# Kernel tuning notes

Measured on AMD Instinct MI355X. Metric: run time of the kernel, lower is better.

Reference implementation:

```python
import jax, jax.numpy as jnp
import numpy as np
import math

H, W = 512, 1024
PS = 2
H_p, W_p = H // PS, W // PS
N = 9
C_IN, C_OUT = 128, 64
GROUPS = 32
B = 2
EPS_GN = 1e-5


def _make_grid():
    # Replicates LatDeform2xDown buffers: centers + sec(lat)-scaled 3x3 offsets.
    pr = np.arange(H_p, dtype=np.float32) * PS + (PS - 1) / 2
    pc = np.arange(W_p, dtype=np.float32) * PS + (PS - 1) / 2
    cy = pr / (H - 1) * 2 - 1
    cx = pc / (W - 1) * 2 - 1
    centers = np.stack([np.broadcast_to(cx[None, :], (H_p, W_p)),
                        np.broadcast_to(cy[:, None], (H_p, W_p))], axis=-1)  # (H_p,W_p,2)
    delta = math.pi / (H - 1)  # drop_south_pole = False
    lat = math.pi / 2 - pr * delta
    sec_max = W / 4.0
    sec = np.clip(1.0 / np.cos(lat), -sec_max, sec_max).astype(np.float32)
    ky, kx = np.meshgrid(np.array([-1.0, 0.0, 1.0], np.float32),
                         np.array([-1.0, 0.0, 1.0], np.float32), indexing='ij')
    kxf, kyf = kx.flatten(), ky.flatten()
    dx = (kxf[None, :] * sec[:, None]) / (W - 1) * 2          # (H_p, 9)
    dy = np.broadcast_to(kyf[None, :], (H_p, N)) / (H - 1) * 2  # (H_p, 9)
    offsets = np.stack([dx, dy], axis=-1)                      # (H_p, 9, 2)
    locs = centers[:, :, None, :] + offsets[:, None, :, :]     # (H_p, W_p, 9, 2)
    return jnp.asarray(locs.reshape(-1, 2).astype(np.float32))


def group_norm(x, gamma, beta, groups, eps=EPS_GN):
    b, c, h, w = x.shape
    xg = x.reshape(b, groups, c // groups, h, w)
    mu = xg.mean(axis=(2, 3, 4), keepdims=True)
    var = ((xg - mu) ** 2).mean(axis=(2, 3, 4), keepdims=True)
    xn = ((xg - mu) * jax.lax.rsqrt(var + eps)).reshape(b, c, h, w)
    return xn * gamma[None, :, None, None] + beta[None, :, None, None]


def setup_inputs() -> dict:
    key = jax.random.key(0)
    ks = jax.random.split(key, 3)
    x = jax.random.normal(ks[0], (B, C_IN, H_p, W_p), dtype=jnp.float32)
    w_conv = jax.random.normal(ks[1], (N * C_OUT, C_IN), dtype=jnp.float32) * 0.02
    w_post = jax.random.normal(ks[2], (C_OUT, C_OUT), dtype=jnp.float32) * 0.05
    return {
        'x': x,
        'grid': _make_grid(),
        'gamma1': jnp.ones((C_IN,), jnp.float32),
        'beta1': jnp.zeros((C_IN,), jnp.float32),
        'w_conv': w_conv,
        'splat_bias': jnp.zeros((C_OUT,), jnp.float32),
        'w_post': w_post,
        'b_post': jnp.zeros((C_OUT,), jnp.float32),
        'gamma2': jnp.ones((C_OUT,), jnp.float32),
        'beta2': jnp.zeros((C_OUT,), jnp.float32),
    }


def reference(x, grid, gamma1, beta1, w_conv, splat_bias, w_post, b_post, gamma2, beta2):
    b = x.shape[0]
    # norm + 1x1 conv (no bias): Wx part of the Wx+b split
    h = group_norm(x, gamma1, beta1, GROUPS)
    vals = jnp.einsum('oc,bchw->bohw', w_conv, h)                 # (B, 9*C, H_p, W_p)
    vals = vals.reshape(b, C_OUT, N, H_p, W_p).transpose(0, 1, 3, 4, 2)
    vals = vals.reshape(b, C_OUT, H_p * W_p * N)                  # (B, C, M)

    # bilinear splat coordinates
    px = (grid[:, 0] + 1.0) * 0.5 * (W - 1)                       # (M,)
    py = (grid[:, 1] + 1.0) * 0.5 * (H - 1)
    x0 = jnp.floor(px).astype(jnp.int32)
    y0 = jnp.floor(py).astype(jnp.int32)
    x1, y1 = x0 + 1, y0 + 1
    fx = px - x0.astype(px.dtype)
    fy = py - y0.astype(py.dtype)
    w00 = (1 - fx) * (1 - fy)
    w01 = (1 - fx) * fy
    w10 = fx * (1 - fy)
    w11 = fx * fy
    x0w = x0 % W
    x1w = x1 % W
    half_W = W // 2

    def polar_wrap(yi, xi):
        past_n = yi < 0
        past_s = yi >= H
        yi = jnp.where(past_n, -yi, yi)
        yi = jnp.where(past_s, 2 * H - yi, yi)
        xi = jnp.where(past_n | past_s, (xi + half_W) % W, xi)
        return jnp.clip(yi, 0, H - 1), xi

    num = jnp.zeros((b, C_OUT, H * W), x.dtype)
    den = jnp.zeros((H * W,), x.dtype)  # identical across batch in the original
    for wt, yi, xi in ((w00, y0, x0w), (w01, y1, x0w), (w10, y0, x1w), (w11, y1, x1w)):
        yi, xi = polar_wrap(yi, xi)
        idx = yi * W + xi                                          # (M,)
        num = num.at[:, :, idx].add(vals * wt[None, None, :])
        den = den.at[idx].add(wt)

    out = num / jnp.clip(den, 1e-8)[None, None, :]
    out = out.reshape(b, C_OUT, H, W) + splat_bias[None, :, None, None]
    # post: 1x1 conv + GroupNorm + exact GELU
    out = jnp.einsum('oc,bchw->bohw', w_post, out) + b_post[None, :, None, None]
    out = group_norm(out, gamma2, beta2, GROUPS)
    return jax.nn.gelu(out, approximate=False)
```

## Files before the change

kernel.cpp:

```cpp
#include <hip/hip_runtime.h>
#include <cstdint>
#include <cstddef>

#define H_   512
#define W_   1024
#define HP_  256
#define WP_  512
#define NTAP 9
#define CIN  128
#define COUT 64
#define HWP  (HP_*WP_)
#define MIDX (HWP*NTAP)
#define HW_  (H_*W_)

typedef __attribute__((ext_vector_type(8))) short bhalf8_t;
typedef __attribute__((ext_vector_type(4))) float floatx4_t;

__device__ __forceinline__ unsigned short f2bf(float f) {
    unsigned u = __float_as_uint(f);
    u += 0x7fffu + ((u >> 16) & 1u);
    return (unsigned short)(u >> 16);
}
__device__ __forceinline__ float bf2f(unsigned short s) {
    return __uint_as_float(((unsigned)s) << 16);
}

__global__ __launch_bounds__(256) void k0_prep(
    const float* __restrict__ w_conv, const float* __restrict__ w_post,
    const float* __restrict__ sbias,  const float* __restrict__ b_post,
    unsigned short* __restrict__ w2, float* __restrict__ sb2,
    float* __restrict__ gnzero ) {
    int idx = blockIdx.x * 256 + threadIdx.x;
    if (idx < 73728) {
        int r = idx >> 7, ci = idx & 127;
        int n = r >> 6, o = r & 63;
        float acc = 0.f;
        #pragma unroll 8
        for (int op = 0; op < 64; ++op)
            acc = fmaf(w_post[o*64 + op], w_conv[(op*9 + n)*128 + ci], acc);
        w2[idx] = f2bf(acc);
    } else if (idx < 73728 + 64) {
        int o = idx - 73728;
        float acc = b_post[o];
        for (int op = 0; op < 64; ++op)
            acc = fmaf(w_post[o*64 + op], sbias[op], acc);
        sb2[o] = acc;
    } else if (idx < 73728 + 64 + 256) {
        gnzero[idx - (73728 + 64)] = 0.f;
    }
}

__global__ __launch_bounds__(256) void k1_stats(const float* __restrict__ x,
                                                float* __restrict__ gnsum1) {
    __shared__ float red[512];
    int bid = blockIdx.x;
    int b = bid >> 8, rem = bid & 255;
    int g = rem >> 3, slice = rem & 7;
    const float4* xp = (const float4*)x + (size_t)(b*CIN + g*4) * (HWP/4) + (size_t)slice*16384;
    float s = 0.f, s2 = 0.f;
    for (int i = threadIdx.x; i < 16384; i += 256) {
        float4 v = xp[i];
        s  += v.x + v.y + v.z + v.w;
        s2 += v.x*v.x + v.y*v.y + v.z*v.z + v.w*v.w;
    }
    red[threadIdx.x] = s; red[256 + threadIdx.x] = s2;
    __syncthreads();
    for (int off = 128; off > 0; off >>= 1) {
        if (threadIdx.x < off) {
            red[threadIdx.x] += red[threadIdx.x + off];
            red[256 + threadIdx.x] += red[256 + threadIdx.x + off];
        }
        __syncthreads();
    }
    if (threadIdx.x == 0) {
        atomicAdd(&gnsum1[(b*32 + g)*2],     red[0]);
        atomicAdd(&gnsum1[(b*32 + g)*2 + 1], red[256]);
    }
}

__global__ void k1b_coef(const float* __restrict__ gnsum1,
                         const float* __restrict__ gamma1, const float* __restrict__ beta1,
                         float* __restrict__ acoef, float* __restrict__ bcoef) {
    int t = threadIdx.x;
    int b = t >> 7, c = t & 127, g = c >> 2;
    float s1 = gnsum1[(b*32+g)*2], s2 = gnsum1[(b*32+g)*2+1];
    const float inv = 1.f / 524288.f;
    float mean = s1 * inv;
    float var  = s2 * inv - mean*mean;
    float rstd = rsqrtf(var + 1e-5f);
    float a = gamma1[c] * rstd;
    acoef[t] = a;
    bcoef[t] = beta1[c] - mean * a;
}

__global__ __launch_bounds__(256) void k2_conv(
    const float* __restrict__ x, const unsigned short* __restrict__ w2,
    const float* __restrict__ acoef, const float* __restrict__ bcoef,
    unsigned short* __restrict__ vals) {
    __shared__ unsigned short As[64*136];
    __shared__ unsigned short Bs[128*136];
    __shared__ unsigned short Cs[128*72];
    int b   = blockIdx.y;
    int tile = blockIdx.x;
    int pr  = tile >> 2, pcb = (tile & 3) << 7;
    int tid = threadIdx.x;

    for (int task = tid; task < 2048; task += 256) {
        int p = task & 127, c0 = (task >> 7) << 3;
        bhalf8_t t8;
        #pragma unroll
        for (int j = 0; j < 8; ++j) {
            int c = c0 + j;
            float xv = x[(size_t)(b*CIN + c)*HWP + (size_t)pr*WP_ + pcb + p];
            float v = fmaf(xv, acoef[b*CIN + c], bcoef[b*CIN + c]);
            t8[j] = (short)f2bf(v);
        }
        *(bhalf8_t*)&Bs[p*136 + c0] = t8;
    }
    __syncthreads();

    int wave = tid >> 6, lane = tid & 63;
    int l15 = lane & 15, lq = lane >> 4;

    bhalf8_t bfr[2][4];
    #pragma unroll
    for (int ptl = 0; ptl < 2; ++ptl) {
        int p = (wave*2 + ptl)*16 + l15;
        #pragma unroll
        for (int ks = 0; ks < 4; ++ks)
            bfr[ptl][ks] = *(const bhalf8_t*)&Bs[p*136 + ks*32 + lq*8];
    }

    for (int n = 0; n < 9; ++n) {
        __syncthreads();
        for (int i = tid; i < 4096; i += 256) {
            int r = i >> 6, cp = i & 63;
            ((unsigned*)As)[r*68 + cp] = ((const unsigned*)w2)[(n*64 + r)*64 + cp];
        }
        __syncthreads();
        floatx4_t acc[2][4] = {};
        #pragma unroll
        for (int ks = 0; ks < 4; ++ks) {
            bhalf8_t af[4];
            #pragma unroll
            for (int rt = 0; rt < 4; ++rt)
                af[rt] = *(const bhalf8_t*)&As[(rt*16 + l15)*136 + ks*32 + lq*8];
            #pragma unroll
            for (int ptl = 0; ptl < 2; ++ptl)
                #pragma unroll
                for (int rt = 0; rt < 4; ++rt)
                    acc[ptl][rt] = __builtin_amdgcn_mfma_f32_16x16x32_bf16(
                        af[rt], bfr[ptl][ks], acc[ptl][rt], 0, 0, 0);
        }
        #pragma unroll
        for (int ptl = 0; ptl < 2; ++ptl) {
            int p = (wave*2 + ptl)*16 + l15;
            #pragma unroll
            for (int rt = 0; rt < 4; ++rt)
                #pragma unroll
                for (int reg = 0; reg < 4; ++reg) {
                    int o = rt*16 + lq*4 + reg;
                    Cs[p*72 + o] = f2bf(acc[ptl][rt][reg]);
                }
        }
        __syncthreads();
        size_t outbase = (size_t)b*HWP + (size_t)pr*WP_ + pcb;
        for (int i = tid; i < 4096; i += 256) {
            int p = i >> 5, o2 = i & 31;
            ((unsigned*)vals)[((outbase + p)*576 + n*64)/2 + o2] = ((const unsigned*)Cs)[p*36 + o2];
        }
    }
}

__global__ __launch_bounds__(256) void k3_gather(
    const float* __restrict__ gridp, const unsigned short* __restrict__ vals,
    const float* __restrict__ sb2g,
    float* __restrict__ out, float* __restrict__ gnsum2) {

    __shared__ float sb2_s[64];
    __shared__ float red[256];

    int tid = threadIdx.x;
    int bx = blockIdx.x;
    int y  = blockIdx.y;
    int b  = blockIdx.z;
    int x  = (bx << 8) + tid;

    if (tid < 64) sb2_s[tid] = sb2g[tid];
    __syncthreads();

    float num[64];
    #pragma unroll
    for (int c = 0; c < 64; ++c) num[c] = 0.f;
    float den = 0.f;

    const float2* g2 = (const float2*)gridp;
    int prc = y >> 1;
    for (int dpr = -1; dpr <= 1; ++dpr) {
        int pr = prc + dpr;
        if (pr < 0 || pr > HP_-1) continue;
        for (int kyi = 0; kyi < 3; ++kyi) {
            float gy = g2[pr*WP_*9 + kyi*3 + 1].y;
            float py = ((gy + 1.0f) * 0.5f) * 511.0f;
            float y0f = floorf(py);
            float fy = py - y0f;
            int y0i = (int)y0f;
            #pragma unroll
            for (int side = 0; side < 2; ++side) {
                int yi = y0i + side;
                bool pn = yi < 0, ps = yi >= H_;
                int yy = pn ? -yi : (ps ? (2*H_ - yi) : yi);
                yy = min(max(yy, 0), H_-1);
                if (yy != y) continue;
                int sh = (pn || ps) ? (W_/2) : 0;
                float wy = side ? fy : (1.0f - fy);
                for (int kxi = 0; kxi < 3; ++kxi) {
                    int n = kyi*3 + kxi;
                    float gx0 = g2[pr*WP_*9 + n].x;
                    float px0 = ((gx0 + 1.0f) * 0.5f) * 1023.0f;
                    int Tt = x - sh - 1;
                    #pragma unroll
                    for (int j = -1; j <= 1; ++j) {
                        float A = ((float)(Tt + j*W_) - px0) * 0.5f;
                        int clo = (int)ceilf(A - 1e-3f);
                        int chi = (int)floorf(A + 1.001f);
                        for (int pc = clo; pc <= chi; ++pc) {
                            if (pc < 0 || pc >= WP_) continue;
                            int m = (pr*WP_ + pc)*9 + n;
                            float2 g = g2[m];
                            float px = ((g.x + 1.0f) * 0.5f) * 1023.0f;
                            float x0f = floorf(px);
                            float fx = px - x0f;
                            int x0i = (int)x0f;
                            int xl = (x0i + 2*W_ + sh) & (W_-1);
                            float w;
                            if (xl == x)                      w = (1.0f - fx) * wy;
                            else if (((xl + 1) & (W_-1)) == x) w = fx * wy;
                            else continue;
                            den += w;
                            const uint4* vp = (const uint4*)(vals + (((size_t)b*MIDX + m) << 6));
                            #pragma unroll
                            for (int q = 0; q < 8; ++q) {
                                uint4 u = vp[q];
                                unsigned uu[4] = {u.x, u.y, u.z, u.w};
                                #pragma unroll
                                for (int e = 0; e < 4; ++e) {
                                    float lo = __uint_as_float(uu[e] << 16);
                                    float hi = __uint_as_float(uu[e] & 0xffff0000u);
                                    num[q*8 + e*2]     = fmaf(w, lo, num[q*8 + e*2]);
                                    num[q*8 + e*2 + 1] = fmaf(w, hi, num[q*8 + e*2 + 1]);
                                }
                            }
                        }
                    }
                }
            }
        }
    }

    float invd = 1.0f / fmaxf(den, 1e-8f);
    size_t obase = ((size_t)b << 25) + ((size_t)y << 10) + (size_t)x;
    #pragma unroll
    for (int c = 0; c < 64; ++c) {
        float v = fmaf(num[c], invd, sb2_s[c]);
        out[obase + ((size_t)c << 19)] = v;
        num[c] = v;
    }

    float st[64];
    #pragma unroll
    for (int g = 0; g < 32; ++g) {
        float a = num[2*g], b2 = num[2*g + 1];
        st[g]      = a + b2;
        st[32 + g] = fmaf(a, a, b2*b2);
    }
    int lane = tid & 63;
    float r32[32];
    { bool hi = (lane & 32) != 0;
      #pragma unroll
      for (int j = 0; j < 32; ++j) {
          float keep = hi ? st[32+j] : st[j];
          float send = hi ? st[j]    : st[32+j];
          r32[j] = keep + __shfl_xor(send, 32, 64);
      } }
    float r16[16];
    { bool hi = (lane & 16) != 0;
      #pragma unroll
      for (int j = 0; j < 16; ++j) {
          float keep = hi ? r32[16+j] : r32[j];
          float send = hi ? r32[j]    : r32[16+j];
          r16[j] = keep + __shfl_xor(send, 16, 64);
      } }
    float r8[8];
    { bool hi = (lane & 8) != 0;
      #pragma unroll
      for (int j = 0; j < 8; ++j) {
          float keep = hi ? r16[8+j] : r16[j];
          float send = hi ? r16[j]   : r16[8+j];
          r8[j] = keep + __shfl_xor(send, 8, 64);
      } }
    float r4[4];
    { bool hi = (lane & 4) != 0;
      #pragma unroll
      for (int j = 0; j < 4; ++j) {
          float keep = hi ? r8[4+j] : r8[j];
          float send = hi ? r8[j]   : r8[4+j];
          r4[j] = keep + __shfl_xor(send, 4, 64);
      } }
    float r2[2];
    { bool hi = (lane & 2) != 0;
      #pragma unroll
      for (int j = 0; j < 2; ++j) {
          float keep = hi ? r4[2+j] : r4[j];
          float send = hi ? r4[j]   : r4[2+j];
          r2[j] = keep + __shfl_xor(send, 2, 64);
      } }
    float r1;
    { bool hi = (lane & 1) != 0;
      float keep = hi ? r2[1] : r2[0];
      float send = hi ? r2[0] : r2[1];
      r1 = keep + __shfl_xor(send, 1, 64);
    }
    red[tid] = r1;
    __syncthreads();
    if (tid < 64) {
        float tot = red[tid] + red[tid + 64] + red[tid + 128] + red[tid + 192];
        int slot = (tid < 32) ? (tid << 1) : (((tid - 32) << 1) + 1);
        atomicAdd(&gnsum2[(b << 6) + slot], tot);
    }
}

__global__ __launch_bounds__(256) void k5_final(
    float* __restrict__ out, const float* __restrict__ gnsum2,
    const float* __restrict__ gamma2, const float* __restrict__ beta2) {
    size_t idx = (size_t)blockIdx.x * 256 + threadIdx.x;
    size_t e8 = idx << 3;
    int b = (int)(e8 >> 25);
    int o = (int)((e8 >> 19) & 63);
    int g = o >> 1;
    float s1 = gnsum2[b*64 + g*2], s2 = gnsum2[b*64 + g*2 + 1];
    const float invn = 1.0f / 1048576.0f;
    float mean = s1 * invn;
    float var  = s2 * invn - mean*mean;
    float rstd = rsqrtf(var + 1e-5f);
    float sc = gamma2[o] * rstd;
    float sf = beta2[o] - mean * sc;
    float4* p0 = (float4*)(out + e8);
    float4 v0 = p0[0], v1 = p0[1];
    float r[8] = {v0.x, v0.y, v0.z, v0.w, v1.x, v1.y, v1.z, v1.w};
    #pragma unroll
    for (int j = 0; j < 8; ++j) {
        float t = fmaf(r[j], sc, sf);
        r[j] = 0.5f * t * (1.0f + erff(t * 0.70710678118654752f));
    }
    p0[0] = make_float4(r[0], r[1], r[2], r[3]);
    p0[1] = make_float4(r[4], r[5], r[6], r[7]);
}

extern "C" void kernel_launch(void* const* d_in, const int* in_sizes, int n_in,
                              void* d_out, int out_size, void* d_ws, size_t ws_size,
                              hipStream_t stream) {
    const float* x      = (const float*)d_in[0];
    const float* gridp  = (const float*)d_in[1];
    const float* gamma1 = (const float*)d_in[2];
    const float* beta1  = (const float*)d_in[3];
    const float* w_conv = (const float*)d_in[4];
    const float* sbias  = (const float*)d_in[5];
    const float* w_post = (const float*)d_in[6];
    const float* b_post = (const float*)d_in[7];
    const float* gamma2 = (const float*)d_in[8];
    const float* beta2  = (const float*)d_in[9];
    float* out = (float*)d_out;

    char* ws = (char*)d_ws;
    unsigned short* w2 = (unsigned short*)(ws);
    float* gnsum1 = (float*)(ws + 147456);
    float* gnsum2 = (float*)(ws + 147968);
    float* acoef  = (float*)(ws + 148480);
    float* bcoef  = (float*)(ws + 149504);
    float* sb2    = (float*)(ws + 150528);
    unsigned short* vals = (unsigned short*)(ws + 150784);

    hipLaunchKernelGGL(k0_prep,  dim3(290),          dim3(256), 0, stream,
                       w_conv, w_post, sbias, b_post, w2, sb2, gnsum1);
    hipLaunchKernelGGL(k1_stats, dim3(512),          dim3(256), 0, stream, x, gnsum1);
    hipLaunchKernelGGL(k1b_coef, dim3(1),            dim3(256), 0, stream,
                       gnsum1, gamma1, beta1, acoef, bcoef);
    hipLaunchKernelGGL(k2_conv,  dim3(1024, 2),      dim3(256), 0, stream,
                       x, w2, acoef, bcoef, vals);
    hipLaunchKernelGGL(k3_gather, dim3(4, 512, 2),   dim3(256), 0, stream,
                       gridp, vals, sb2, out, gnsum2);
    hipLaunchKernelGGL(k5_final, dim3(32768),        dim3(256), 0, stream,
                       out, gnsum2, gamma2, beta2);
}
```

Baseline: 886.7 us.

## Fold GroupNorm affine into per-batch conv weights and bias, read weights from global

The first GroupNorm's scale is folded into a per-batch bf16 copy of the fused conv weight, and its shift becomes a per-output bias computed by a new small kernel. The conv kernel then converts raw x straight to bf16 with packed conversion instructions and seeds its accumulators with that bias. It also drops the LDS staging of weights (and two barriers per tap) in favour of direct global/L2 loads of A fragments. The costs are one extra launch and a small per-batch weight buffer, plus a slightly different rounding path, since the normalisation is now applied in the weights rather than to the bf16-rounded activations.

```diff
diff --git a/kernel.cpp b/kernel.cpp
--- a/kernel.cpp
+++ b/kernel.cpp
@@ -21,14 +21,16 @@
     u += 0x7fffu + ((u >> 16) & 1u);
     return (unsigned short)(u >> 16);
 }
-__device__ __forceinline__ float bf2f(unsigned short s) {
-    return __uint_as_float(((unsigned)s) << 16);
+__device__ __forceinline__ unsigned cvt_pk_bf16(float lo, float hi) {
+    unsigned r;
+    asm("v_cvt_pk_bf16_f32 %0, %1, %2" : "=v"(r) : "v"(lo), "v"(hi));
+    return r;
 }
 
 __global__ __launch_bounds__(256) void k0_prep(
     const float* __restrict__ w_conv, const float* __restrict__ w_post,
     const float* __restrict__ sbias,  const float* __restrict__ b_post,
-    unsigned short* __restrict__ w2, float* __restrict__ sb2,
+    float* __restrict__ wfold, float* __restrict__ sb2,
     float* __restrict__ gnzero ) {
     int idx = blockIdx.x * 256 + threadIdx.x;
     if (idx < 73728) {
@@ -38,7 +40,7 @@
         #pragma unroll 8
         for (int op = 0; op < 64; ++op)
             acc = fmaf(w_post[o*64 + op], w_conv[(op*9 + n)*128 + ci], acc);
-        w2[idx] = f2bf(acc);
+        wfold[idx] = acc;
     } else if (idx < 73728 + 64) {
         int o = idx - 73728;
         float acc = b_post[o];
@@ -93,11 +95,29 @@
     bcoef[t] = beta1[c] - mean * a;
 }
 
+__global__ __launch_bounds__(256) void k1c_scale(
+    const float* __restrict__ wfold, const float* __restrict__ acoef,
+    const float* __restrict__ bcoef,
+    unsigned short* __restrict__ w2b, float* __restrict__ vb) {
+    int b = blockIdx.y;
+    int idx = blockIdx.x * 256 + threadIdx.x;
+    if (idx < 73728) {
+        int c = idx & 127;
+        w2b[b*73728 + idx] = f2bf(wfold[idx] * acoef[b*128 + c]);
+    } else if (idx < 73728 + 576) {
+        int r = idx - 73728;
+        float acc = 0.f;
+        #pragma unroll 8
+        for (int c = 0; c < 128; ++c)
+            acc = fmaf(wfold[r*128 + c], bcoef[b*128 + c], acc);
+        vb[b*576 + r] = acc;
+    }
+}
+
 __global__ __launch_bounds__(256) void k2_conv(
-    const float* __restrict__ x, const unsigned short* __restrict__ w2,
-    const float* __restrict__ acoef, const float* __restrict__ bcoef,
+    const float* __restrict__ x, const unsigned short* __restrict__ w2b,
+    const float* __restrict__ vb,
     unsigned short* __restrict__ vals) {
-    __shared__ unsigned short As[64*136];
     __shared__ unsigned short Bs[128*136];
     __shared__ unsigned short Cs[128*72];
     int b   = blockIdx.y;
@@ -107,15 +127,21 @@
 
     for (int task = tid; task < 2048; task += 256) {
         int p = task & 127, c0 = (task >> 7) << 3;
-        bhalf8_t t8;
-        #pragma unroll
-        for (int j = 0; j < 8; ++j) {
-            int c = c0 + j;
-            float xv = x[(size_t)(b*CIN + c)*HWP + (size_t)pr*WP_ + pcb + p];
-            float v = fmaf(xv, acoef[b*CIN + c], bcoef[b*CIN + c]);
-            t8[j] = (short)f2bf(v);
-        }
-        *(bhalf8_t*)&Bs[p*136 + c0] = t8;
+        const float* xp = &x[(size_t)(b*CIN + c0)*HWP + (size_t)pr*WP_ + pcb + p];
+        float v0 = xp[0];
+        float v1 = xp[HWP];
+        float v2 = xp[2*HWP];
+        float v3 = xp[3*HWP];
+        float v4 = xp[4*HWP];
+        float v5 = xp[5*HWP];
+        float v6 = xp[6*HWP];
+        float v7 = xp[7*HWP];
+        uint4 t;
+        t.x = cvt_pk_bf16(v0, v1);
+        t.y = cvt_pk_bf16(v2, v3);
+        t.z = cvt_pk_bf16(v4, v5);
+        t.w = cvt_pk_bf16(v6, v7);
+        *(uint4*)&Bs[p*136 + c0] = t;
     }
     __syncthreads();
 
@@ -131,20 +157,23 @@
             bfr[ptl][ks] = *(const bhalf8_t*)&Bs[p*136 + ks*32 + lq*8];
     }
 
+    const unsigned short* wb = w2b + (size_t)b*73728;
+    const float* vbb = vb + b*576;
+
     for (int n = 0; n < 9; ++n) {
-        __syncthreads();
-        for (int i = tid; i < 4096; i += 256) {
-            int r = i >> 6, cp = i & 63;
-            ((unsigned*)As)[r*68 + cp] = ((const unsigned*)w2)[(n*64 + r)*64 + cp];
-        }
-        __syncthreads();
-        floatx4_t acc[2][4] = {};
+        floatx4_t acc[2][4];
+        #pragma unroll
+        for (int rt = 0; rt < 4; ++rt) {
+            float4 vbv = *(const float4*)&vbb[n*64 + rt*16 + lq*4];
+            floatx4_t a0; a0[0] = vbv.x; a0[1] = vbv.y; a0[2] = vbv.z; a0[3] = vbv.w;
+            acc[0][rt] = a0; acc[1][rt] = a0;
+        }
         #pragma unroll
         for (int ks = 0; ks < 4; ++ks) {
             bhalf8_t af[4];
             #pragma unroll
             for (int rt = 0; rt < 4; ++rt)
-                af[rt] = *(const bhalf8_t*)&As[(rt*16 + l15)*136 + ks*32 + lq*8];
+                af[rt] = *(const bhalf8_t*)&wb[(n*64 + rt*16 + l15)*128 + ks*32 + lq*8];
             #pragma unroll
             for (int ptl = 0; ptl < 2; ++ptl)
                 #pragma unroll
@@ -152,16 +181,17 @@
                     acc[ptl][rt] = __builtin_amdgcn_mfma_f32_16x16x32_bf16(
                         af[rt], bfr[ptl][ks], acc[ptl][rt], 0, 0, 0);
         }
+        __syncthreads();
         #pragma unroll
         for (int ptl = 0; ptl < 2; ++ptl) {
             int p = (wave*2 + ptl)*16 + l15;
             #pragma unroll
-            for (int rt = 0; rt < 4; ++rt)
-                #pragma unroll
-                for (int reg = 0; reg < 4; ++reg) {
-                    int o = rt*16 + lq*4 + reg;
-                    Cs[p*72 + o] = f2bf(acc[ptl][rt][reg]);
-                }
+            for (int rt = 0; rt < 4; ++rt) {
+                uint2 d;
+                d.x = cvt_pk_bf16(acc[ptl][rt][0], acc[ptl][rt][1]);
+                d.y = cvt_pk_bf16(acc[ptl][rt][2], acc[ptl][rt][3]);
+                *(uint2*)&Cs[p*72 + rt*16 + lq*4] = d;
+            }
         }
         __syncthreads();
         size_t outbase = (size_t)b*HWP + (size_t)pr*WP_ + pcb;
@@ -373,21 +403,25 @@
     float* out = (float*)d_out;
 
     char* ws = (char*)d_ws;
-    unsigned short* w2 = (unsigned short*)(ws);
-    float* gnsum1 = (float*)(ws + 147456);
-    float* gnsum2 = (float*)(ws + 147968);
-    float* acoef  = (float*)(ws + 148480);
-    float* bcoef  = (float*)(ws + 149504);
-    float* sb2    = (float*)(ws + 150528);
-    unsigned short* vals = (unsigned short*)(ws + 150784);
+    float* wfold  = (float*)(ws);
+    unsigned short* w2b = (unsigned short*)(ws + 294912);
+    float* vb     = (float*)(ws + 589824);
+    float* gnsum1 = (float*)(ws + 594432);
+    float* gnsum2 = (float*)(ws + 594944);
+    float* acoef  = (float*)(ws + 595456);
+    float* bcoef  = (float*)(ws + 596480);
+    float* sb2    = (float*)(ws + 597504);
+    unsigned short* vals = (unsigned short*)(ws + 597760);
 
     hipLaunchKernelGGL(k0_prep,  dim3(290),          dim3(256), 0, stream,
-                       w_conv, w_post, sbias, b_post, w2, sb2, gnsum1);
+                       w_conv, w_post, sbias, b_post, wfold, sb2, gnsum1);
     hipLaunchKernelGGL(k1_stats, dim3(512),          dim3(256), 0, stream, x, gnsum1);
     hipLaunchKernelGGL(k1b_coef, dim3(1),            dim3(256), 0, stream,
                        gnsum1, gamma1, beta1, acoef, bcoef);
+    hipLaunchKernelGGL(k1c_scale, dim3(291, 2),      dim3(256), 0, stream,
+                       wfold, acoef, bcoef, w2b, vb);
     hipLaunchKernelGGL(k2_conv,  dim3(1024, 2),      dim3(256), 0, stream,
-                       x, w2, acoef, bcoef, vals);
+                       x, w2b, vb, vals);
     hipLaunchKernelGGL(k3_gather, dim3(4, 512, 2),   dim3(256), 0, stream,
                        gridp, vals, sb2, out, gnsum2);
     hipLaunchKernelGGL(k5_final, dim3(32768),        dim3(256), 0, stream,
```

Result: faster. 848.1 us (-4.3%).
